# Performance work log

Hardware: AMD Instinct MI355X
Metric: run time of the kernel (lower is better)

Reference implementation:

```python
import jax, jax.numpy as jnp
import numpy as np

N, E, F, K = 50000, 320000, 256, 2

def setup_inputs() -> dict:
    key = jax.random.key(0)
    k0, k1, k2, k3 = jax.random.split(key, 4)
    x = jax.random.normal(k0, (N, F), dtype=jnp.float32)
    edge_index = jax.random.randint(k1, (2, E), 0, N, dtype=jnp.int64)
    s = 1.0 / np.sqrt(F)
    init_weight = jax.random.uniform(k2, (K, F, F), jnp.float32, -s, s)
    root_weight = jax.random.uniform(k3, (K, F, F), jnp.float32, -s, s)
    bias = jnp.zeros((K, 1, F), dtype=jnp.float32)
    return {"x": x, "edge_index": edge_index, "init_weight": init_weight,
            "root_weight": root_weight, "bias": bias}

def reference(x, edge_index, init_weight, root_weight, bias):
    src = edge_index[0]
    dst = edge_index[1]
    n = x.shape[0]
    # gcn_norm without self-loops: deg over target index, sym normalization
    deg = jax.ops.segment_sum(jnp.ones((E,), x.dtype), dst, num_segments=n)
    dinv = jnp.where(deg > 0, jax.lax.rsqrt(jnp.maximum(deg, 1.0)), 0.0)
    w = dinv[src] * dinv[dst]                                   # [E]
    # ARMAConv, num_layers=1: out = act(A_hat @ (x W_k) + x V_k + b_k), mean over K
    h = jnp.einsum('nf,kfg->kng', x, init_weight)               # [K,N,F]
    msg = h[:, src, :] * w[None, :, None]                       # [K,E,F]
    agg = jax.vmap(lambda m: jax.ops.segment_sum(m, dst, num_segments=n))(msg)  # [K,N,F]
    root = jnp.einsum('nf,kfg->kng', x, root_weight)            # [K,N,F]
    arma = jax.nn.relu(agg + root + bias).mean(axis=0)          # [N,F]
    return x + jax.nn.relu(arma)
```

## Files before the change

### kernel.cpp

```cpp
#include <hip/hip_runtime.h>

#define NN 50000
#define NE 320000
#define FF 256
#define SCAN_B 196
#define DEG_B  1250
#define XCVT_B 12500
#define BPREP_B 128

typedef short short8 __attribute__((ext_vector_type(8)));
typedef float f32x4 __attribute__((ext_vector_type(4)));
typedef unsigned short us4 __attribute__((ext_vector_type(4)));

static __device__ __forceinline__ unsigned short f2bf(float f) {
    union { float f; unsigned u; } v; v.f = f;
    unsigned r = v.u + 0x7FFFu + ((v.u >> 16) & 1u);
    return (unsigned short)(r >> 16);
}
static __device__ __forceinline__ float bf2f(unsigned short h) {
    return __uint_as_float((unsigned)h << 16);
}

__global__ __launch_bounds__(256)
void k_pre(const int* __restrict__ ei, int* __restrict__ deg,
           const float* __restrict__ x, unsigned short* __restrict__ Ab,
           const float* __restrict__ wi, const float* __restrict__ wr,
           unsigned short* __restrict__ Bp) {
    const int b = blockIdx.x;
    if (b < DEG_B) {
        int e = b * 256 + threadIdx.x;
        if (e < NE) atomicAdd(&deg[ei[NE + e]], 1);
    } else if (b < DEG_B + XCVT_B) {
        int t = (b - DEG_B) * 256 + threadIdx.x;
        if (t < NN * 64) {
            int n = t >> 6, q = t & 63;
            float4 v = *reinterpret_cast<const float4*>(&x[(size_t)n * FF + q * 4]);
            us4 o = {f2bf(v.x), f2bf(v.y), f2bf(v.z), f2bf(v.w)};
            char* rowp = (char*)(Ab + (size_t)n * 512);
            *reinterpret_cast<us4*>(rowp + ((512 + q * 8) ^ ((n & 7) << 4))) = o;
        }
    } else {
        int t = (b - DEG_B - XCVT_B) * 256 + threadIdx.x;
        int l = t & 63;
        int fb = t >> 6;
        int kc = fb >> 5;
        int cf = fb & 31;
        int col = cf * 16 + (l & 15);
        int kpart = col >> 8;
        int g = col & 255;
        int K0 = kc * 32 + (l >> 4) * 8;
        unsigned short* dst = Bp + (size_t)fb * 512 + (size_t)l * 8;
        #pragma unroll
        for (int e = 0; e < 8; ++e) {
            int K = K0 + e;
            const float* srcp = (K < 256) ? wi : wr;
            float v = srcp[(size_t)kpart * 65536 + (size_t)(K & 255) * 256 + g];
            dst[e] = f2bf(v);
        }
    }
}

__global__ void k_scan1(const int* __restrict__ deg, int* __restrict__ bsum) {
    __shared__ int s[256];
    int i = blockIdx.x * 256 + threadIdx.x;
    s[threadIdx.x] = (i < NN) ? deg[i] : 0;
    __syncthreads();
    for (int d = 128; d > 0; d >>= 1) {
        if (threadIdx.x < d) s[threadIdx.x] += s[threadIdx.x + d];
        __syncthreads();
    }
    if (threadIdx.x == 0) bsum[blockIdx.x] = s[0];
}

__global__ void k_scan3(const int* __restrict__ deg, const int* __restrict__ bsum,
                        int* __restrict__ off, int* __restrict__ cur,
                        float* __restrict__ dinv) {
    __shared__ int sb[256];
    __shared__ int s[256];
    const int t = threadIdx.x;
    int bv = (t < SCAN_B) ? bsum[t] : 0;
    sb[t] = bv;
    __syncthreads();
    for (int d = 1; d < 256; d <<= 1) {
        int u = (t >= d) ? sb[t - d] : 0;
        __syncthreads();
        sb[t] += u;
        __syncthreads();
    }
    const int boff = sb[blockIdx.x] - bsum[blockIdx.x];
    int i = blockIdx.x * 256 + t;
    int v = (i < NN) ? deg[i] : 0;
    s[t] = v;
    __syncthreads();
    for (int d = 1; d < 256; d <<= 1) {
        int u = (t >= d) ? s[t - d] : 0;
        __syncthreads();
        s[t] += u;
        __syncthreads();
    }
    if (i < NN) {
        int excl = boff + s[t] - v;
        off[i] = excl;
        cur[i] = excl;
        dinv[i] = v > 0 ? rsqrtf((float)v) : 0.f;
    }
}

__global__ void k_fill(const int* __restrict__ ei, int* __restrict__ cur,
                       int* __restrict__ csr_src) {
    int e = blockIdx.x * blockDim.x + threadIdx.x;
    if (e < NE) {
        int dst = ei[NE + e];
        int pos = atomicAdd(&cur[dst], 1);
        csr_src[pos] = ei[e];
    }
}

__global__ __launch_bounds__(256)
void k_agg(const int* __restrict__ off, const int* __restrict__ deg,
           const int* __restrict__ csr_src, const float* __restrict__ dinv,
           unsigned short* __restrict__ Ab) {
    int wid = (blockIdx.x * blockDim.x + threadIdx.x) >> 6;
    if (wid >= NN) return;
    int lane = threadIdx.x & 63;
    int start = off[wid];
    int d = deg[wid];
    float di = dinv[wid];
    const char* base = (const char*)Ab;
    const int lb = 512 + lane * 8;
    float4 acc = make_float4(0.f, 0.f, 0.f, 0.f);
    int e = 0;
    for (; e + 4 <= d; e += 4) {
        int s0 = csr_src[start + e + 0];
        int s1 = csr_src[start + e + 1];
        int s2 = csr_src[start + e + 2];
        int s3 = csr_src[start + e + 3];
        us4 v0 = *reinterpret_cast<const us4*>(base + (size_t)s0 * 1024 + (lb ^ ((s0 & 7) << 4)));
        us4 v1 = *reinterpret_cast<const us4*>(base + (size_t)s1 * 1024 + (lb ^ ((s1 & 7) << 4)));
        us4 v2 = *reinterpret_cast<const us4*>(base + (size_t)s2 * 1024 + (lb ^ ((s2 & 7) << 4)));
        us4 v3 = *reinterpret_cast<const us4*>(base + (size_t)s3 * 1024 + (lb ^ ((s3 & 7) << 4)));
        float w0 = di * dinv[s0], w1 = di * dinv[s1], w2 = di * dinv[s2], w3 = di * dinv[s3];
        acc.x = fmaf(w0, bf2f(v0[0]), fmaf(w1, bf2f(v1[0]), fmaf(w2, bf2f(v2[0]), fmaf(w3, bf2f(v3[0]), acc.x))));
        acc.y = fmaf(w0, bf2f(v0[1]), fmaf(w1, bf2f(v1[1]), fmaf(w2, bf2f(v2[1]), fmaf(w3, bf2f(v3[1]), acc.y))));
        acc.z = fmaf(w0, bf2f(v0[2]), fmaf(w1, bf2f(v1[2]), fmaf(w2, bf2f(v2[2]), fmaf(w3, bf2f(v3[2]), acc.z))));
        acc.w = fmaf(w0, bf2f(v0[3]), fmaf(w1, bf2f(v1[3]), fmaf(w2, bf2f(v2[3]), fmaf(w3, bf2f(v3[3]), acc.w))));
    }
    for (; e < d; ++e) {
        int s0 = csr_src[start + e];
        us4 v0 = *reinterpret_cast<const us4*>(base + (size_t)s0 * 1024 + (lb ^ ((s0 & 7) << 4)));
        float w0 = di * dinv[s0];
        acc.x = fmaf(w0, bf2f(v0[0]), acc.x);
        acc.y = fmaf(w0, bf2f(v0[1]), acc.y);
        acc.z = fmaf(w0, bf2f(v0[2]), acc.z);
        acc.w = fmaf(w0, bf2f(v0[3]), acc.w);
    }
    char* rowp = (char*)(Ab + (size_t)wid * 512);
    us4 o = {f2bf(acc.x), f2bf(acc.y), f2bf(acc.z), f2bf(acc.w)};
    *reinterpret_cast<us4*>(rowp + ((lane * 8) ^ ((wid & 7) << 4))) = o;
}

#define LOADB(dst, kc_)                                                           \
    {                                                                             \
        dst[0] = *reinterpret_cast<const short8*>(bpb + (kc_) * 32768 + (2 * w + 0) * 1024);        \
        dst[1] = *reinterpret_cast<const short8*>(bpb + (kc_) * 32768 + (2 * w + 1) * 1024);        \
        dst[2] = *reinterpret_cast<const short8*>(bpb + (kc_) * 32768 + (16 + 2 * w) * 1024);       \
        dst[3] = *reinterpret_cast<const short8*>(bpb + (kc_) * 32768 + (17 + 2 * w) * 1024);       \
    }
#define LOADA1K(dst, ab, kc2_)                                                    \
    {                                                                             \
        _Pragma("unroll")                                                         \
        for (int rf = 0; rf < 4; ++rf)                                            \
            dst[rf] = *reinterpret_cast<const short8*>((ab) + rf * 16384 + (kc2_) * 128); \
    }
#define MFMA4(aset, bset)                                                         \
    {                                                                             \
        _Pragma("unroll")                                                         \
        for (int rf = 0; rf < 4; ++rf)                                            \
            _Pragma("unroll")                                                     \
            for (int c = 0; c < 4; ++c)                                           \
                acc[rf][c] = __builtin_amdgcn_mfma_f32_16x16x32_bf16(aset[rf], bset[c], acc[rf][c], 0, 0, 0); \
    }

__global__ __launch_bounds__(512, 4)
void k_mm(const unsigned short* __restrict__ Ab, const unsigned short* __restrict__ Bp,
          const float* __restrict__ bias, float* __restrict__ out) {
    __shared__ char smem[65536];

    const int l = threadIdx.x & 63;
    const int w = threadIdx.x >> 6;
    const int row0 = blockIdx.x * 64;

    {
        const char* base = (const char*)Ab;
        #pragma unroll
        for (int j = 0; j < 8; ++j) {
            int rl = j * 8 + w;
            int rsrc = row0 + rl; if (rsrc >= NN) rsrc = NN - 1;
            const char* gp = base + (size_t)rsrc * 1024 + l * 16;
            __builtin_amdgcn_global_load_lds(
                (const __attribute__((address_space(1))) void*)gp,
                (__attribute__((address_space(3))) void*)(smem + rl * 1024),
                16, 0, 0);
        }
    }
    __syncthreads();

    f32x4 acc[4][4];
    #pragma unroll
    for (int i = 0; i < 4; ++i)
        #pragma unroll
        for (int j = 0; j < 4; ++j) acc[i][j] = (f32x4){0.f, 0.f, 0.f, 0.f};

    const int p = l & 7, q = l >> 4;
    const char* abase0 = smem + (l & 15) * 1024 + ((p >> 2) << 6) + ((q ^ (p & 3)) << 4);
    const char* abase1 = smem + (((size_t)(abase0 - smem)) ^ 64);
    const char* bpb = (const char*)(Bp + (size_t)l * 8);

    short8 b0[4], b1[4], a[4];
    LOADB(b0, 0)
    #pragma unroll 1
    for (int kc2 = 0; kc2 < 7; ++kc2) {
        LOADA1K(a, abase0, kc2)
        LOADB(b1, 2 * kc2 + 1)
        MFMA4(a, b0)
        LOADA1K(a, abase1, kc2)
        LOADB(b0, 2 * kc2 + 2)
        MFMA4(a, b1)
    }
    {
        LOADA1K(a, abase0, 7)
        LOADB(b1, 15)
        MFMA4(a, b0)
        LOADA1K(a, abase1, 7)
        MFMA4(a, b1)
    }

    __syncthreads();

    #pragma unroll
    for (int rf = 0; rf < 4; ++rf) {
        const int rl0 = rf * 16 + (l >> 4) * 4;
        #pragma unroll
        for (int j = 0; j < 4; ++j) {
            int rl = rl0 + j;
            int r = row0 + rl;
            if (r >= NN) continue;
            int sw = (rl & 7) << 4;
            #pragma unroll
            for (int c = 0; c < 2; ++c) {
                int gg = w * 32 + c * 16 + (l & 15);
                unsigned short xb =
                    *reinterpret_cast<const unsigned short*>(&smem[rl * 1024 + ((512 + gg * 2) ^ sw)]);
                float xv = bf2f(xb);
                float c0 = acc[rf][c][j] + bias[gg];
                float c1 = acc[rf][c + 2][j] + bias[256 + gg];
                float arma = 0.5f * (fmaxf(c0, 0.f) + fmaxf(c1, 0.f));
                out[(size_t)r * FF + gg] = xv + fmaxf(arma, 0.f);
            }
        }
    }
}

extern "C" void kernel_launch(void* const* d_in, const int* in_sizes, int n_in,
                              void* d_out, int out_size, void* d_ws, size_t ws_size,
                              hipStream_t stream) {
    const float* x    = (const float*)d_in[0];
    const int*   ei   = (const int*)d_in[1];
    const float* wi   = (const float*)d_in[2];
    const float* wr   = (const float*)d_in[3];
    const float* bias = (const float*)d_in[4];
    float* out = (float*)d_out;

    int*   deg     = (int*)d_ws;
    int*   off     = deg + NN;
    int*   cur     = off + NN;
    int*   csr_src = cur + NN;
    float* dinv    = (float*)(csr_src + NE);
    int*   bsum    = (int*)(dinv + NN);
    unsigned short* Bp = (unsigned short*)(bsum + SCAN_B);
    unsigned short* Ab = (unsigned short*)d_out;

    hipMemsetAsync(deg, 0, NN * sizeof(int), stream);

    k_pre  <<<DEG_B + XCVT_B + BPREP_B, 256, 0, stream>>>(ei, deg, x, Ab, wi, wr, Bp);
    k_scan1<<<SCAN_B, 256, 0, stream>>>(deg, bsum);
    k_scan3<<<SCAN_B, 256, 0, stream>>>(deg, bsum, off, cur, dinv);
    k_fill <<<(NE + 255) / 256, 256, 0, stream>>>(ei, cur, csr_src);
    k_agg  <<<(NN * 64 + 255) / 256, 256, 0, stream>>>(off, deg, csr_src, dinv, Ab);
    k_mm   <<<(NN + 63) / 64, 512, 0, stream>>>(Ab, Bp, bias, out);
}
```

Baseline: 130.0 us.

## Fuse scan and CSR fill into one grid-barrier kernel; widen aggregation loads

Merges the two scan kernels and the CSR fill kernel into a single persistent kernel of 196 blocks that synchronises through atomic grid barriers. This removes two kernel launches and their gaps. Separately, the aggregation kernel now handles two nodes per wavefront, each lane loading 8 bf16 values (16 bytes) instead of 4, which halves the wavefront count and widens the memory transactions. The grid barrier assumes all 196 blocks are co-resident, and the fill phase now runs on far fewer threads, which may slow the atomic scatter.

New measurement: 165.9 us. 27.6% more time.

```diff
diff --git a/kernel.cpp b/kernel.cpp
--- a/kernel.cpp
+++ b/kernel.cpp
@@ -11,6 +11,7 @@
 typedef short short8 __attribute__((ext_vector_type(8)));
 typedef float f32x4 __attribute__((ext_vector_type(4)));
 typedef unsigned short us4 __attribute__((ext_vector_type(4)));
+typedef unsigned short us8 __attribute__((ext_vector_type(8)));
 
 static __device__ __forceinline__ unsigned short f2bf(float f) {
     union { float f; unsigned u; } v; v.f = f;
@@ -60,25 +61,38 @@
     }
 }
 
-__global__ void k_scan1(const int* __restrict__ deg, int* __restrict__ bsum) {
+__device__ __forceinline__ void gbar(int* bar, int idx) {
+    __syncthreads();
+    if (threadIdx.x == 0) {
+        __threadfence();
+        atomicAdd(&bar[idx], 1);
+        while (__hip_atomic_load(&bar[idx], __ATOMIC_ACQUIRE, __HIP_MEMORY_SCOPE_AGENT) < (int)gridDim.x) {}
+        __threadfence();
+    }
+    __syncthreads();
+}
+
+__global__ __launch_bounds__(256)
+void k_csr(const int* __restrict__ ei, const int* __restrict__ deg,
+           int* __restrict__ bsum, int* __restrict__ off, int* __restrict__ cur,
+           float* __restrict__ dinv, int* __restrict__ csr_src, int* __restrict__ bar) {
     __shared__ int s[256];
-    int i = blockIdx.x * 256 + threadIdx.x;
-    s[threadIdx.x] = (i < NN) ? deg[i] : 0;
+    __shared__ int sb[256];
+    const int t = threadIdx.x;
+    const int b = blockIdx.x;
+    const int i = b * 256 + t;
+    const int v = (i < NN) ? deg[i] : 0;
+
+    s[t] = v;
     __syncthreads();
     for (int d = 128; d > 0; d >>= 1) {
-        if (threadIdx.x < d) s[threadIdx.x] += s[threadIdx.x + d];
-        __syncthreads();
-    }
-    if (threadIdx.x == 0) bsum[blockIdx.x] = s[0];
-}
-
-__global__ void k_scan3(const int* __restrict__ deg, const int* __restrict__ bsum,
-                        int* __restrict__ off, int* __restrict__ cur,
-                        float* __restrict__ dinv) {
-    __shared__ int sb[256];
-    __shared__ int s[256];
-    const int t = threadIdx.x;
-    int bv = (t < SCAN_B) ? bsum[t] : 0;
+        if (t < d) s[t] += s[t + d];
+        __syncthreads();
+    }
+    if (t == 0) __hip_atomic_store(&bsum[b], s[0], __ATOMIC_RELEASE, __HIP_MEMORY_SCOPE_AGENT);
+    gbar(bar, 0);
+
+    int bv = (t < SCAN_B) ? __hip_atomic_load(&bsum[t], __ATOMIC_ACQUIRE, __HIP_MEMORY_SCOPE_AGENT) : 0;
     sb[t] = bv;
     __syncthreads();
     for (int d = 1; d < 256; d <<= 1) {
@@ -87,9 +101,7 @@
         sb[t] += u;
         __syncthreads();
     }
-    const int boff = sb[blockIdx.x] - bsum[blockIdx.x];
-    int i = blockIdx.x * 256 + t;
-    int v = (i < NN) ? deg[i] : 0;
+    const int boff = (b > 0) ? sb[b - 1] : 0;
     s[t] = v;
     __syncthreads();
     for (int d = 1; d < 256; d <<= 1) {
@@ -101,15 +113,12 @@
     if (i < NN) {
         int excl = boff + s[t] - v;
         off[i] = excl;
-        cur[i] = excl;
+        __hip_atomic_store(&cur[i], excl, __ATOMIC_RELEASE, __HIP_MEMORY_SCOPE_AGENT);
         dinv[i] = v > 0 ? rsqrtf((float)v) : 0.f;
     }
-}
-
-__global__ void k_fill(const int* __restrict__ ei, int* __restrict__ cur,
-                       int* __restrict__ csr_src) {
-    int e = blockIdx.x * blockDim.x + threadIdx.x;
-    if (e < NE) {
+    gbar(bar, 1);
+
+    for (int e = b * 256 + t; e < NE; e += SCAN_B * 256) {
         int dst = ei[NE + e];
         int pos = atomicAdd(&cur[dst], 1);
         csr_src[pos] = ei[e];
@@ -121,42 +130,46 @@
            const int* __restrict__ csr_src, const float* __restrict__ dinv,
            unsigned short* __restrict__ Ab) {
     int wid = (blockIdx.x * blockDim.x + threadIdx.x) >> 6;
-    if (wid >= NN) return;
-    int lane = threadIdx.x & 63;
-    int start = off[wid];
-    int d = deg[wid];
-    float di = dinv[wid];
+    if (wid >= NN / 2) return;
+    int l = threadIdx.x & 63;
+    int n = wid * 2 + (l >> 5);
+    int start = off[n];
+    int d = deg[n];
+    float di = dinv[n];
     const char* base = (const char*)Ab;
-    const int lb = 512 + lane * 8;
-    float4 acc = make_float4(0.f, 0.f, 0.f, 0.f);
+    const int lq = (l & 31) * 16;
+    const int lb = 512 + lq;
+    float acc[8];
+    #pragma unroll
+    for (int j = 0; j < 8; ++j) acc[j] = 0.f;
     int e = 0;
     for (; e + 4 <= d; e += 4) {
         int s0 = csr_src[start + e + 0];
         int s1 = csr_src[start + e + 1];
         int s2 = csr_src[start + e + 2];
         int s3 = csr_src[start + e + 3];
-        us4 v0 = *reinterpret_cast<const us4*>(base + (size_t)s0 * 1024 + (lb ^ ((s0 & 7) << 4)));
-        us4 v1 = *reinterpret_cast<const us4*>(base + (size_t)s1 * 1024 + (lb ^ ((s1 & 7) << 4)));
-        us4 v2 = *reinterpret_cast<const us4*>(base + (size_t)s2 * 1024 + (lb ^ ((s2 & 7) << 4)));
-        us4 v3 = *reinterpret_cast<const us4*>(base + (size_t)s3 * 1024 + (lb ^ ((s3 & 7) << 4)));
+        us8 v0 = *reinterpret_cast<const us8*>(base + (size_t)s0 * 1024 + (lb ^ ((s0 & 7) << 4)));
+        us8 v1 = *reinterpret_cast<const us8*>(base + (size_t)s1 * 1024 + (lb ^ ((s1 & 7) << 4)));
+        us8 v2 = *reinterpret_cast<const us8*>(base + (size_t)s2 * 1024 + (lb ^ ((s2 & 7) << 4)));
+        us8 v3 = *reinterpret_cast<const us8*>(base + (size_t)s3 * 1024 + (lb ^ ((s3 & 7) << 4)));
         float w0 = di * dinv[s0], w1 = di * dinv[s1], w2 = di * dinv[s2], w3 = di * dinv[s3];
-        acc.x = fmaf(w0, bf2f(v0[0]), fmaf(w1, bf2f(v1[0]), fmaf(w2, bf2f(v2[0]), fmaf(w3, bf2f(v3[0]), acc.x))));
-        acc.y = fmaf(w0, bf2f(v0[1]), fmaf(w1, bf2f(v1[1]), fmaf(w2, bf2f(v2[1]), fmaf(w3, bf2f(v3[1]), acc.y))));
-        acc.z = fmaf(w0, bf2f(v0[2]), fmaf(w1, bf2f(v1[2]), fmaf(w2, bf2f(v2[2]), fmaf(w3, bf2f(v3[2]), acc.z))));
-        acc.w = fmaf(w0, bf2f(v0[3]), fmaf(w1, bf2f(v1[3]), fmaf(w2, bf2f(v2[3]), fmaf(w3, bf2f(v3[3]), acc.w))));
+        #pragma unroll
+        for (int j = 0; j < 8; ++j)
+            acc[j] = fmaf(w0, bf2f(v0[j]), fmaf(w1, bf2f(v1[j]),
+                     fmaf(w2, bf2f(v2[j]), fmaf(w3, bf2f(v3[j]), acc[j]))));
     }
     for (; e < d; ++e) {
         int s0 = csr_src[start + e];
-        us4 v0 = *reinterpret_cast<const us4*>(base + (size_t)s0 * 1024 + (lb ^ ((s0 & 7) << 4)));
+        us8 v0 = *reinterpret_cast<const us8*>(base + (size_t)s0 * 1024 + (lb ^ ((s0 & 7) << 4)));
         float w0 = di * dinv[s0];
-        acc.x = fmaf(w0, bf2f(v0[0]), acc.x);
-        acc.y = fmaf(w0, bf2f(v0[1]), acc.y);
-        acc.z = fmaf(w0, bf2f(v0[2]), acc.z);
-        acc.w = fmaf(w0, bf2f(v0[3]), acc.w);
-    }
-    char* rowp = (char*)(Ab + (size_t)wid * 512);
-    us4 o = {f2bf(acc.x), f2bf(acc.y), f2bf(acc.z), f2bf(acc.w)};
-    *reinterpret_cast<us4*>(rowp + ((lane * 8) ^ ((wid & 7) << 4))) = o;
+        #pragma unroll
+        for (int j = 0; j < 8; ++j)
+            acc[j] = fmaf(w0, bf2f(v0[j]), acc[j]);
+    }
+    us8 o;
+    #pragma unroll
+    for (int j = 0; j < 8; ++j) o[j] = f2bf(acc[j]);
+    *reinterpret_cast<us8*>((char*)Ab + (size_t)n * 1024 + (lq ^ ((n & 7) << 4))) = o;
 }
 
 #define LOADB(dst, kc_)                                                           \
@@ -272,7 +285,8 @@
     float* out = (float*)d_out;
 
     int*   deg     = (int*)d_ws;
-    int*   off     = deg + NN;
+    int*   bar     = deg + NN;
+    int*   off     = bar + 2;
     int*   cur     = off + NN;
     int*   csr_src = cur + NN;
     float* dinv    = (float*)(csr_src + NE);
@@ -280,12 +294,10 @@
     unsigned short* Bp = (unsigned short*)(bsum + SCAN_B);
     unsigned short* Ab = (unsigned short*)d_out;
 
-    hipMemsetAsync(deg, 0, NN * sizeof(int), stream);
-
-    k_pre  <<<DEG_B + XCVT_B + BPREP_B, 256, 0, stream>>>(ei, deg, x, Ab, wi, wr, Bp);
-    k_scan1<<<SCAN_B, 256, 0, stream>>>(deg, bsum);
-    k_scan3<<<SCAN_B, 256, 0, stream>>>(deg, bsum, off, cur, dinv);
-    k_fill <<<(NE + 255) / 256, 256, 0, stream>>>(ei, cur, csr_src);
-    k_agg  <<<(NN * 64 + 255) / 256, 256, 0, stream>>>(off, deg, csr_src, dinv, Ab);
-    k_mm   <<<(NN + 63) / 64, 512, 0, stream>>>(Ab, Bp, bias, out);
-}
+    hipMemsetAsync(deg, 0, (NN + 2) * sizeof(int), stream);
+
+    k_pre<<<DEG_B + XCVT_B + BPREP_B, 256, 0, stream>>>(ei, deg, x, Ab, wi, wr, Bp);
+    k_csr<<<SCAN_B, 256, 0, stream>>>(ei, deg, bsum, off, cur, dinv, csr_src, bar);
+    k_agg<<<(NN / 2 * 64 + 255) / 256, 256, 0, stream>>>(off, deg, csr_src, dinv, Ab);
+    k_mm <<<(NN + 63) / 64, 512, 0, stream>>>(Ab, Bp, bias, out);
+}
```
